# Kernel tuning notes

Measured on AMD Instinct MI355X. Metric: run time of the kernel, lower is better.

Reference implementation:

```python
import jax, jax.numpy as jnp
import numpy as np
from jax import lax

WINDOW_SIZE = 11
SIGMA = 1.5
C1 = 0.01 ** 2
C2 = 0.03 ** 2


def _make_window():
    xs = np.arange(WINDOW_SIZE) - WINDOW_SIZE // 2
    g = np.exp(-(xs.astype(np.float32) ** 2) / (2.0 * SIGMA ** 2))
    g = g / g.sum()
    w2d = np.outer(g, g).astype(np.float32)  # (ws, ws)
    return jnp.asarray(w2d)[None, None, :, :]  # (O=1, I=1, ws, ws)


def _blur(x, window):
    pad = WINDOW_SIZE // 2
    return lax.conv_general_dilated(
        x, window,
        window_strides=(1, 1),
        padding=[(pad, pad), (pad, pad)],
        dimension_numbers=("NCHW", "OIHW", "NCHW"),
    )


def setup_inputs() -> dict:
    key = jax.random.key(0)
    k1, k2 = jax.random.split(key)
    shape = (64, 1, 512, 512)
    img1 = jax.random.uniform(k1, shape, dtype=jnp.float32)
    img2 = jax.random.uniform(k2, shape, dtype=jnp.float32)
    return {"img1": img1, "img2": img2}


def reference(img1, img2):
    window = _make_window()
    mu1 = _blur(img1, window)
    mu2 = _blur(img2, window)
    mu1_sq = mu1 * mu1
    mu2_sq = mu2 * mu2
    mu1_mu2 = mu1 * mu2
    sigma1_sq = _blur(img1 * img1, window) - mu1_sq
    sigma2_sq = _blur(img2 * img2, window) - mu2_sq
    sigma12 = _blur(img1 * img2, window) - mu1_mu2
    ssim_map = ((2.0 * mu1_mu2 + C1) * (2.0 * sigma12 + C2)) / (
        (mu1_sq + mu2_sq + C1) * (sigma1_sq + sigma2_sq + C2)
    )
    return ssim_map.mean()  # size_average=True
```

## Files before the change

kernel.cpp:

```cpp
#include <hip/hip_runtime.h>

#define IMG 512
#define HALO 5
#define BAND 16
#define NB 8
#define RING 26

#define W0 1.0283800e-03f
#define W1 7.5987582e-03f
#define W2 3.6000773e-02f
#define W3 1.0936070e-01f
#define W4 2.1300553e-01f
#define W5 2.6601172e-01f

typedef float f2 __attribute__((ext_vector_type(2)));

__device__ __forceinline__ f2 pkfma(f2 a, f2 b, f2 c) {
    return __builtin_elementwise_fma(a, b, c);
}

#define LGKM_BARRIER() asm volatile("s_waitcnt lgkmcnt(0)\n\ts_barrier" ::: "memory")

__global__ __launch_bounds__(256, 5)
void ssim_main(const float* __restrict__ img1, const float* __restrict__ img2,
               float* __restrict__ part)
{
    const float Wt[11] = {W0,W1,W2,W3,W4,W5,W4,W3,W2,W1,W0};
    constexpr float C1 = 1.0e-4f;
    constexpr float C2 = 9.0e-4f;

    __shared__ float4 sH[RING][64];
    __shared__ float  sRed[4];

    const int bx      = blockIdx.x;
    const int n       = bx >> 5;
    const int stripe  = (bx >> 2) & 7;
    const int quarter = bx & 3;
    const int gx0     = stripe << 6;
    const int base    = quarter << 7;
    const int tid     = threadIdx.x;
    const bool edge   = (stripe == 0) | (stripe == 7);

    const float* __restrict__ base1 = img1 + (size_t)n * IMG * IMG;
    const float* __restrict__ base2 = img2 + (size_t)n * IMG * IMG;

    float acc = 0.0f;

    auto loadRowP = [&](const float* r1, const float* r2, bool rok, int gcb,
                        float4* px, float4* py) {
        #pragma unroll
        for (int t = 0; t < 5; ++t) {
            int gc = gcb - 8 + (t << 2);
            bool ok = rok && (gc >= 0) && (gc < IMG);
            px[t] = ok ? ((const float4*)r1)[t] : make_float4(0.f,0.f,0.f,0.f);
            py[t] = ok ? ((const float4*)r2)[t] : make_float4(0.f,0.f,0.f,0.f);
        }
    };

    auto horizStore = [&](const float4* px, const float4* py, int slot, int cg) {
        f2 m[4]  = {f2{0.f,0.f},f2{0.f,0.f},f2{0.f,0.f},f2{0.f,0.f}};
        f2 t2[4] = {f2{0.f,0.f},f2{0.f,0.f},f2{0.f,0.f},f2{0.f,0.f}};
        #pragma unroll
        for (int t = 0; t < 5; ++t) {
            #pragma unroll
            for (int e = 0; e < 4; ++e) {
                const int j = (t << 2) + e;
                if (j < 3 || j > 16) continue;
                const float x = (e==0) ? px[t].x : (e==1) ? px[t].y : (e==2) ? px[t].z : px[t].w;
                const float y = (e==0) ? py[t].x : (e==1) ? py[t].y : (e==2) ? py[t].z : py[t].w;
                const f2 v  = {x, y};
                const f2 s2 = {fmaf(x, x, y*y), x*y};
                #pragma unroll
                for (int o = 0; o < 4; ++o) {
                    const int k = j - 3 - o;
                    if (0 <= k && k <= 10) {
                        const f2 w = {Wt[k], Wt[k]};
                        m[o]  = pkfma(w, v,  m[o]);
                        t2[o] = pkfma(w, s2, t2[o]);
                    }
                }
            }
        }
        const int c4 = cg << 2;
        #pragma unroll
        for (int o = 0; o < 4; ++o) {
            const int wc = (c4 + o) ^ cg;
            sH[slot][wc] = make_float4(m[o].x, m[o].y, t2[o].x, t2[o].y);
        }
    };

    for (int task = tid; task < RING * 16; task += 256) {
        const int i   = task >> 4;
        const int cg  = task & 15;
        const int gr  = base - HALO + i;
        const int gcb = gx0 + (cg << 2);
        const float* r1 = base1 + (ptrdiff_t)gr * IMG + gcb - 8;
        const float* r2 = base2 + (ptrdiff_t)gr * IMG + gcb - 8;
        float4 px[5], py[5];
        if (!edge && gr >= 0) {
            #pragma unroll
            for (int t = 0; t < 5; ++t) {
                px[t] = ((const float4*)r1)[t];
                py[t] = ((const float4*)r2)[t];
            }
        } else {
            loadRowP(r1, r2, gr >= 0, gcb, px, py);
        }
        horizStore(px, py, i, cg);
    }

    const int rr  = tid >> 4;
    const int cgs = tid & 15;
    const int gcb = gx0 + (cgs << 2);
    const float* p1 = base1 + (ptrdiff_t)(base + 21 + rr) * IMG + gcb - 8;
    const float* p2 = base2 + (ptrdiff_t)(base + 21 + rr) * IMG + gcb - 8;

    const int col  = tid & 63;
    const int rcol = col ^ (col >> 2);
    const int wv   = __builtin_amdgcn_readfirstlane(tid >> 6);

    int sb = 0;
    for (int b = 0; b < NB; ++b) {
        float4 px[5], py[5];
        const bool pf = (b + 1 < NB);
        if (pf) {
            const bool rowsafe = (quarter < 3) | (b < NB - 2);
            if (rowsafe & (!edge)) {
                #pragma unroll
                for (int t = 0; t < 5; ++t) {
                    px[t] = ((const float4*)p1)[t];
                    py[t] = ((const float4*)p2)[t];
                }
            } else {
                const int gr = base + (b << 4) + 21 + rr;
                loadRowP(p1, p2, (unsigned)gr < (unsigned)IMG, gcb, px, py);
            }
        }

        LGKM_BARRIER();

        {
            const int d0 = sb + (wv << 2);
            f2 ma[4] = {f2{0.f,0.f},f2{0.f,0.f},f2{0.f,0.f},f2{0.f,0.f}};
            f2 sa[4] = {f2{0.f,0.f},f2{0.f,0.f},f2{0.f,0.f},f2{0.f,0.f}};
            #pragma unroll
            for (int i = 0; i < 14; ++i) {
                int s = d0 + i;
                s -= (s >= RING) ? RING : 0;
                const float4 q = sH[s][rcol];
                const f2 v = {q.x, q.y};
                const f2 u = {q.z, q.w};
                #pragma unroll
                for (int o = 0; o < 4; ++o) {
                    const int k = i - o;
                    if (0 <= k && k <= 10) {
                        const f2 w = {Wt[k], Wt[k]};
                        ma[o] = pkfma(w, v, ma[o]);
                        sa[o] = pkfma(w, u, sa[o]);
                    }
                }
            }
            #pragma unroll
            for (int o = 0; o < 4; ++o) {
                const f2 m   = ma[o];
                const f2 tt  = sa[o];
                const f2 msq = m * m;
                const float mu12  = m.x * m.y;
                const float musum = msq.x + msq.y;
                const float g12 = tt.y - mu12;
                const float gs  = tt.x - musum;
                const float num = fmaf(2.f, mu12, C1) * fmaf(2.f, g12, C2);
                const float den = (musum + C1) * (gs + C2);
                acc = fmaf(num, __builtin_amdgcn_rcpf(den), acc);
            }
        }

        LGKM_BARRIER();

        if (pf) {
            int t = sb + rr;
            t -= (t >= RING) ? RING : 0;
            horizStore(px, py, t, cgs);
            p1 += BAND * IMG;
            p2 += BAND * IMG;
        }
        sb += BAND;
        sb -= (sb >= RING) ? RING : 0;
    }

    #pragma unroll
    for (int off = 32; off > 0; off >>= 1)
        acc += __shfl_down(acc, off, 64);
    if ((tid & 63) == 0) sRed[tid >> 6] = acc;
    LGKM_BARRIER();
    if (tid == 0) part[bx] = sRed[0] + sRed[1] + sRed[2] + sRed[3];
}

__global__ void ssim_finalize(const float* __restrict__ part, float* __restrict__ out)
{
    __shared__ double sD[4];
    double s = 0.0;
    const int t = threadIdx.x;
    for (int i = t; i < 2048; i += 256) s += (double)part[i];
    #pragma unroll
    for (int off = 32; off > 0; off >>= 1)
        s += __shfl_down(s, off, 64);
    if ((t & 63) == 0) sD[t >> 6] = s;
    __syncthreads();
    if (t == 0) out[0] = (float)((sD[0] + sD[1] + sD[2] + sD[3]) * (1.0 / 16777216.0));
}

extern "C" void kernel_launch(void* const* d_in, const int* in_sizes, int n_in,
                              void* d_out, int out_size, void* d_ws, size_t ws_size,
                              hipStream_t stream)
{
    const float* img1 = (const float*)d_in[0];
    const float* img2 = (const float*)d_in[1];
    float* out  = (float*)d_out;
    float* part = (float*)d_ws;

    ssim_main<<<2048, 256, 0, stream>>>(img1, img2, part);
    ssim_finalize<<<1, 256, 0, stream>>>(part, out);
}
```

Baseline: 170.1 us.

## Double-buffer row prefetch registers to load two bands ahead

Row data is now prefetched into two alternating register sets (A/B), so each band's global loads are issued about two iterations before use rather than one. The first steady-state load is issued before the initial ring fill to overlap with it. The main loop is unrolled by two so the buffers alternate. Launch bounds drop from 5 to 4 blocks per CU to fit the extra registers, which lowers occupancy in exchange for more memory-latency hiding.

```diff
diff --git a/kernel.cpp b/kernel.cpp
--- a/kernel.cpp
+++ b/kernel.cpp
@@ -21,7 +21,7 @@
 
 #define LGKM_BARRIER() asm volatile("s_waitcnt lgkmcnt(0)\n\ts_barrier" ::: "memory")
 
-__global__ __launch_bounds__(256, 5)
+__global__ __launch_bounds__(256, 4)
 void ssim_main(const float* __restrict__ img1, const float* __restrict__ img2,
                float* __restrict__ part)
 {
@@ -46,11 +46,11 @@
 
     float acc = 0.0f;
 
-    auto loadRowP = [&](const float* r1, const float* r2, bool rok, int gcb,
+    auto loadRowP = [&](const float* r1, const float* r2, bool rok, int gcb_,
                         float4* px, float4* py) {
         #pragma unroll
         for (int t = 0; t < 5; ++t) {
-            int gc = gcb - 8 + (t << 2);
+            int gc = gcb_ - 8 + (t << 2);
             bool ok = rok && (gc >= 0) && (gc < IMG);
             px[t] = ok ? ((const float4*)r1)[t] : make_float4(0.f,0.f,0.f,0.f);
             py[t] = ok ? ((const float4*)r2)[t] : make_float4(0.f,0.f,0.f,0.f);
@@ -89,13 +89,81 @@
         }
     };
 
+    const int rr  = tid >> 4;
+    const int cgs = tid & 15;
+    const int gcb = gx0 + (cgs << 2);
+
+    const float* pA1 = base1 + (ptrdiff_t)(base + 21 + rr) * IMG + gcb - 8;
+    const float* pA2 = base2 + (ptrdiff_t)(base + 21 + rr) * IMG + gcb - 8;
+    const float* pB1 = pA1 + BAND * IMG;
+    const float* pB2 = pA2 + BAND * IMG;
+
+    float4 pxA[5], pyA[5], pxB[5], pyB[5];
+
+    auto loadSteady = [&](float4* px, float4* py, const float* q1, const float* q2, int k) {
+        const bool rowsafe = (quarter < 3) | (k < NB - 2);
+        if (rowsafe & (!edge)) {
+            #pragma unroll
+            for (int t = 0; t < 5; ++t) {
+                px[t] = ((const float4*)q1)[t];
+                py[t] = ((const float4*)q2)[t];
+            }
+        } else {
+            const int gr = base + (k << 4) + 21 + rr;
+            loadRowP(q1, q2, (unsigned)gr < (unsigned)IMG, gcb, px, py);
+        }
+    };
+
+    const int col  = tid & 63;
+    const int rcol = col ^ (col >> 2);
+    const int wv   = __builtin_amdgcn_readfirstlane(tid >> 6);
+
+    auto vertical = [&](int sb_) {
+        const int d0 = sb_ + (wv << 2);
+        f2 ma[4] = {f2{0.f,0.f},f2{0.f,0.f},f2{0.f,0.f},f2{0.f,0.f}};
+        f2 sa[4] = {f2{0.f,0.f},f2{0.f,0.f},f2{0.f,0.f},f2{0.f,0.f}};
+        #pragma unroll
+        for (int i = 0; i < 14; ++i) {
+            int s = d0 + i;
+            s -= (s >= RING) ? RING : 0;
+            const float4 q = sH[s][rcol];
+            const f2 v = {q.x, q.y};
+            const f2 u = {q.z, q.w};
+            #pragma unroll
+            for (int o = 0; o < 4; ++o) {
+                const int k = i - o;
+                if (0 <= k && k <= 10) {
+                    const f2 w = {Wt[k], Wt[k]};
+                    ma[o] = pkfma(w, v, ma[o]);
+                    sa[o] = pkfma(w, u, sa[o]);
+                }
+            }
+        }
+        #pragma unroll
+        for (int o = 0; o < 4; ++o) {
+            const f2 m   = ma[o];
+            const f2 tt  = sa[o];
+            const f2 msq = m * m;
+            const float mu12  = m.x * m.y;
+            const float musum = msq.x + msq.y;
+            const float g12 = tt.y - mu12;
+            const float gs  = tt.x - musum;
+            const float num = fmaf(2.f, mu12, C1) * fmaf(2.f, g12, C2);
+            const float den = (musum + C1) * (gs + C2);
+            acc = fmaf(num, __builtin_amdgcn_rcpf(den), acc);
+        }
+    };
+
+    loadSteady(pxA, pyA, pA1, pA2, 0);
+    pA1 += 2 * BAND * IMG;  pA2 += 2 * BAND * IMG;
+
     for (int task = tid; task < RING * 16; task += 256) {
         const int i   = task >> 4;
         const int cg  = task & 15;
         const int gr  = base - HALO + i;
-        const int gcb = gx0 + (cg << 2);
-        const float* r1 = base1 + (ptrdiff_t)gr * IMG + gcb - 8;
-        const float* r2 = base2 + (ptrdiff_t)gr * IMG + gcb - 8;
+        const int gcb2 = gx0 + (cg << 2);
+        const float* r1 = base1 + (ptrdiff_t)gr * IMG + gcb2 - 8;
+        const float* r2 = base2 + (ptrdiff_t)gr * IMG + gcb2 - 8;
         float4 px[5], py[5];
         if (!edge && gr >= 0) {
             #pragma unroll
@@ -104,88 +172,40 @@
                 py[t] = ((const float4*)r2)[t];
             }
         } else {
-            loadRowP(r1, r2, gr >= 0, gcb, px, py);
+            loadRowP(r1, r2, gr >= 0, gcb2, px, py);
         }
         horizStore(px, py, i, cg);
     }
 
-    const int rr  = tid >> 4;
-    const int cgs = tid & 15;
-    const int gcb = gx0 + (cgs << 2);
-    const float* p1 = base1 + (ptrdiff_t)(base + 21 + rr) * IMG + gcb - 8;
-    const float* p2 = base2 + (ptrdiff_t)(base + 21 + rr) * IMG + gcb - 8;
-
-    const int col  = tid & 63;
-    const int rcol = col ^ (col >> 2);
-    const int wv   = __builtin_amdgcn_readfirstlane(tid >> 6);
-
     int sb = 0;
-    for (int b = 0; b < NB; ++b) {
-        float4 px[5], py[5];
-        const bool pf = (b + 1 < NB);
-        if (pf) {
-            const bool rowsafe = (quarter < 3) | (b < NB - 2);
-            if (rowsafe & (!edge)) {
-                #pragma unroll
-                for (int t = 0; t < 5; ++t) {
-                    px[t] = ((const float4*)p1)[t];
-                    py[t] = ((const float4*)p2)[t];
-                }
-            } else {
-                const int gr = base + (b << 4) + 21 + rr;
-                loadRowP(p1, p2, (unsigned)gr < (unsigned)IMG, gcb, px, py);
-            }
-        }
-
-        LGKM_BARRIER();
-
+    for (int b = 0; b < NB; b += 2) {
+        if (b + 1 <= NB - 2) {
+            loadSteady(pxB, pyB, pB1, pB2, b + 1);
+            pB1 += 2 * BAND * IMG;  pB2 += 2 * BAND * IMG;
+        }
+        LGKM_BARRIER();
+        vertical(sb);
+        LGKM_BARRIER();
         {
-            const int d0 = sb + (wv << 2);
-            f2 ma[4] = {f2{0.f,0.f},f2{0.f,0.f},f2{0.f,0.f},f2{0.f,0.f}};
-            f2 sa[4] = {f2{0.f,0.f},f2{0.f,0.f},f2{0.f,0.f},f2{0.f,0.f}};
-            #pragma unroll
-            for (int i = 0; i < 14; ++i) {
-                int s = d0 + i;
-                s -= (s >= RING) ? RING : 0;
-                const float4 q = sH[s][rcol];
-                const f2 v = {q.x, q.y};
-                const f2 u = {q.z, q.w};
-                #pragma unroll
-                for (int o = 0; o < 4; ++o) {
-                    const int k = i - o;
-                    if (0 <= k && k <= 10) {
-                        const f2 w = {Wt[k], Wt[k]};
-                        ma[o] = pkfma(w, v, ma[o]);
-                        sa[o] = pkfma(w, u, sa[o]);
-                    }
-                }
-            }
-            #pragma unroll
-            for (int o = 0; o < 4; ++o) {
-                const f2 m   = ma[o];
-                const f2 tt  = sa[o];
-                const f2 msq = m * m;
-                const float mu12  = m.x * m.y;
-                const float musum = msq.x + msq.y;
-                const float g12 = tt.y - mu12;
-                const float gs  = tt.x - musum;
-                const float num = fmaf(2.f, mu12, C1) * fmaf(2.f, g12, C2);
-                const float den = (musum + C1) * (gs + C2);
-                acc = fmaf(num, __builtin_amdgcn_rcpf(den), acc);
-            }
-        }
-
-        LGKM_BARRIER();
-
-        if (pf) {
             int t = sb + rr;
             t -= (t >= RING) ? RING : 0;
-            horizStore(px, py, t, cgs);
-            p1 += BAND * IMG;
-            p2 += BAND * IMG;
-        }
-        sb += BAND;
-        sb -= (sb >= RING) ? RING : 0;
+            horizStore(pxA, pyA, t, cgs);
+        }
+        sb += BAND; sb -= (sb >= RING) ? RING : 0;
+
+        if (b + 2 <= NB - 2) {
+            loadSteady(pxA, pyA, pA1, pA2, b + 2);
+            pA1 += 2 * BAND * IMG;  pA2 += 2 * BAND * IMG;
+        }
+        LGKM_BARRIER();
+        vertical(sb);
+        LGKM_BARRIER();
+        if (b + 1 <= NB - 2) {
+            int t = sb + rr;
+            t -= (t >= RING) ? RING : 0;
+            horizStore(pxB, pyB, t, cgs);
+        }
+        sb += BAND; sb -= (sb >= RING) ? RING : 0;
     }
 
     #pragma unroll
```

After: 643.8 us. 3.78x slower.

## Prefetch rows two bands ahead and compute horizontal blur before barrier

Applied to the files above, without the earlier changes.

The steady-state global load is issued one band earlier, and the first band's load now happens before the prologue. The horizontal blur of the prefetched row is computed in registers before the vertical pass, so only the LDS store stays after the second barrier. This hides more global-memory latency behind compute and shortens the time between barriers. In exchange it holds more live registers (raw rows plus blurred results), so occupancy drops from 5 to 4 blocks per SIMD via launch bounds.

```diff
diff --git a/kernel.cpp b/kernel.cpp
--- a/kernel.cpp
+++ b/kernel.cpp
@@ -21,7 +21,7 @@
 
 #define LGKM_BARRIER() asm volatile("s_waitcnt lgkmcnt(0)\n\ts_barrier" ::: "memory")
 
-__global__ __launch_bounds__(256, 5)
+__global__ __launch_bounds__(256, 4)
 void ssim_main(const float* __restrict__ img1, const float* __restrict__ img2,
                float* __restrict__ part)
 {
@@ -46,20 +46,20 @@
 
     float acc = 0.0f;
 
-    auto loadRowP = [&](const float* r1, const float* r2, bool rok, int gcb,
+    auto loadRowP = [&](const float* r1, const float* r2, bool rok, int gcb_,
                         float4* px, float4* py) {
         #pragma unroll
         for (int t = 0; t < 5; ++t) {
-            int gc = gcb - 8 + (t << 2);
+            int gc = gcb_ - 8 + (t << 2);
             bool ok = rok && (gc >= 0) && (gc < IMG);
             px[t] = ok ? ((const float4*)r1)[t] : make_float4(0.f,0.f,0.f,0.f);
             py[t] = ok ? ((const float4*)r2)[t] : make_float4(0.f,0.f,0.f,0.f);
         }
     };
 
-    auto horizStore = [&](const float4* px, const float4* py, int slot, int cg) {
-        f2 m[4]  = {f2{0.f,0.f},f2{0.f,0.f},f2{0.f,0.f},f2{0.f,0.f}};
-        f2 t2[4] = {f2{0.f,0.f},f2{0.f,0.f},f2{0.f,0.f},f2{0.f,0.f}};
+    auto hblurRegs = [&](const float4* px, const float4* py, f2* m, f2* t2) {
+        #pragma unroll
+        for (int o = 0; o < 4; ++o) { m[o] = f2{0.f,0.f}; t2[o] = f2{0.f,0.f}; }
         #pragma unroll
         for (int t = 0; t < 5; ++t) {
             #pragma unroll
@@ -81,6 +81,11 @@
                 }
             }
         }
+    };
+
+    auto horizStore = [&](const float4* px, const float4* py, int slot, int cg) {
+        f2 m[4], t2[4];
+        hblurRegs(px, py, m, t2);
         const int c4 = cg << 2;
         #pragma unroll
         for (int o = 0; o < 4; ++o) {
@@ -88,104 +93,118 @@
             sH[slot][wc] = make_float4(m[o].x, m[o].y, t2[o].x, t2[o].y);
         }
     };
+
+    const int rr  = tid >> 4;
+    const int cgs = tid & 15;
+    const int gcb = gx0 + (cgs << 2);
+
+    const float* p1 = base1 + (ptrdiff_t)(base + 21 + rr) * IMG + gcb - 8;
+    const float* p2 = base2 + (ptrdiff_t)(base + 21 + rr) * IMG + gcb - 8;
+
+    float4 px[5], py[5];
+    f2 bm[4], bt[4];
+
+    auto loadSteady = [&](int k) {
+        const bool rowsafe = (quarter < 3) | (k < NB - 2);
+        if (rowsafe & (!edge)) {
+            #pragma unroll
+            for (int t = 0; t < 5; ++t) {
+                px[t] = ((const float4*)p1)[t];
+                py[t] = ((const float4*)p2)[t];
+            }
+        } else {
+            const int gr = base + (k << 4) + 21 + rr;
+            loadRowP(p1, p2, (unsigned)gr < (unsigned)IMG, gcb, px, py);
+        }
+        p1 += BAND * IMG;
+        p2 += BAND * IMG;
+    };
+
+    const int col  = tid & 63;
+    const int rcol = col ^ (col >> 2);
+    const int wv   = __builtin_amdgcn_readfirstlane(tid >> 6);
+
+    auto vertical = [&](int sb_) {
+        const int d0 = sb_ + (wv << 2);
+        f2 ma[4] = {f2{0.f,0.f},f2{0.f,0.f},f2{0.f,0.f},f2{0.f,0.f}};
+        f2 sa[4] = {f2{0.f,0.f},f2{0.f,0.f},f2{0.f,0.f},f2{0.f,0.f}};
+        #pragma unroll
+        for (int i = 0; i < 14; ++i) {
+            int s = d0 + i;
+            s -= (s >= RING) ? RING : 0;
+            const float4 q = sH[s][rcol];
+            const f2 v = {q.x, q.y};
+            const f2 u = {q.z, q.w};
+            #pragma unroll
+            for (int o = 0; o < 4; ++o) {
+                const int k = i - o;
+                if (0 <= k && k <= 10) {
+                    const f2 w = {Wt[k], Wt[k]};
+                    ma[o] = pkfma(w, v, ma[o]);
+                    sa[o] = pkfma(w, u, sa[o]);
+                }
+            }
+        }
+        #pragma unroll
+        for (int o = 0; o < 4; ++o) {
+            const f2 m   = ma[o];
+            const f2 tt  = sa[o];
+            const f2 msq = m * m;
+            const float mu12  = m.x * m.y;
+            const float musum = msq.x + msq.y;
+            const float g12 = tt.y - mu12;
+            const float gs  = tt.x - musum;
+            const float num = fmaf(2.f, mu12, C1) * fmaf(2.f, g12, C2);
+            const float den = (musum + C1) * (gs + C2);
+            acc = fmaf(num, __builtin_amdgcn_rcpf(den), acc);
+        }
+    };
+
+    loadSteady(0);
 
     for (int task = tid; task < RING * 16; task += 256) {
         const int i   = task >> 4;
         const int cg  = task & 15;
         const int gr  = base - HALO + i;
-        const int gcb = gx0 + (cg << 2);
-        const float* r1 = base1 + (ptrdiff_t)gr * IMG + gcb - 8;
-        const float* r2 = base2 + (ptrdiff_t)gr * IMG + gcb - 8;
-        float4 px[5], py[5];
+        const int gcb2 = gx0 + (cg << 2);
+        const float* r1 = base1 + (ptrdiff_t)gr * IMG + gcb2 - 8;
+        const float* r2 = base2 + (ptrdiff_t)gr * IMG + gcb2 - 8;
+        float4 qx[5], qy[5];
         if (!edge && gr >= 0) {
             #pragma unroll
             for (int t = 0; t < 5; ++t) {
-                px[t] = ((const float4*)r1)[t];
-                py[t] = ((const float4*)r2)[t];
+                qx[t] = ((const float4*)r1)[t];
+                qy[t] = ((const float4*)r2)[t];
             }
         } else {
-            loadRowP(r1, r2, gr >= 0, gcb, px, py);
-        }
-        horizStore(px, py, i, cg);
+            loadRowP(r1, r2, gr >= 0, gcb2, qx, qy);
+        }
+        horizStore(qx, qy, i, cg);
     }
-
-    const int rr  = tid >> 4;
-    const int cgs = tid & 15;
-    const int gcb = gx0 + (cgs << 2);
-    const float* p1 = base1 + (ptrdiff_t)(base + 21 + rr) * IMG + gcb - 8;
-    const float* p2 = base2 + (ptrdiff_t)(base + 21 + rr) * IMG + gcb - 8;
-
-    const int col  = tid & 63;
-    const int rcol = col ^ (col >> 2);
-    const int wv   = __builtin_amdgcn_readfirstlane(tid >> 6);
 
     int sb = 0;
     for (int b = 0; b < NB; ++b) {
-        float4 px[5], py[5];
-        const bool pf = (b + 1 < NB);
-        if (pf) {
-            const bool rowsafe = (quarter < 3) | (b < NB - 2);
-            if (rowsafe & (!edge)) {
-                #pragma unroll
-                for (int t = 0; t < 5; ++t) {
-                    px[t] = ((const float4*)p1)[t];
-                    py[t] = ((const float4*)p2)[t];
-                }
-            } else {
-                const int gr = base + (b << 4) + 21 + rr;
-                loadRowP(p1, p2, (unsigned)gr < (unsigned)IMG, gcb, px, py);
-            }
+        if (b <= NB - 2) {
+            hblurRegs(px, py, bm, bt);
+            if (b <= NB - 3)
+                loadSteady(b + 1);
         }
 
         LGKM_BARRIER();
-
-        {
-            const int d0 = sb + (wv << 2);
-            f2 ma[4] = {f2{0.f,0.f},f2{0.f,0.f},f2{0.f,0.f},f2{0.f,0.f}};
-            f2 sa[4] = {f2{0.f,0.f},f2{0.f,0.f},f2{0.f,0.f},f2{0.f,0.f}};
-            #pragma unroll
-            for (int i = 0; i < 14; ++i) {
-                int s = d0 + i;
-                s -= (s >= RING) ? RING : 0;
-                const float4 q = sH[s][rcol];
-                const f2 v = {q.x, q.y};
-                const f2 u = {q.z, q.w};
-                #pragma unroll
-                for (int o = 0; o < 4; ++o) {
-                    const int k = i - o;
-                    if (0 <= k && k <= 10) {
-                        const f2 w = {Wt[k], Wt[k]};
-                        ma[o] = pkfma(w, v, ma[o]);
-                        sa[o] = pkfma(w, u, sa[o]);
-                    }
-                }
-            }
-            #pragma unroll
-            for (int o = 0; o < 4; ++o) {
-                const f2 m   = ma[o];
-                const f2 tt  = sa[o];
-                const f2 msq = m * m;
-                const float mu12  = m.x * m.y;
-                const float musum = msq.x + msq.y;
-                const float g12 = tt.y - mu12;
-                const float gs  = tt.x - musum;
-                const float num = fmaf(2.f, mu12, C1) * fmaf(2.f, g12, C2);
-                const float den = (musum + C1) * (gs + C2);
-                acc = fmaf(num, __builtin_amdgcn_rcpf(den), acc);
-            }
-        }
-
+        vertical(sb);
         LGKM_BARRIER();
 
-        if (pf) {
+        if (b <= NB - 2) {
             int t = sb + rr;
             t -= (t >= RING) ? RING : 0;
-            horizStore(px, py, t, cgs);
-            p1 += BAND * IMG;
-            p2 += BAND * IMG;
-        }
-        sb += BAND;
-        sb -= (sb >= RING) ? RING : 0;
+            const int c4 = cgs << 2;
+            #pragma unroll
+            for (int o = 0; o < 4; ++o) {
+                const int wc = (c4 + o) ^ cgs;
+                sH[t][wc] = make_float4(bm[o].x, bm[o].y, bt[o].x, bt[o].y);
+            }
+        }
+        sb += BAND; sb -= (sb >= RING) ? RING : 0;
     }
 
     #pragma unroll
```

New measurement: 176.7 us. 3.9% more time.
